# Performance work log

Hardware: AMD Instinct MI355X
Metric: run time of the kernel (lower is better)

Reference implementation:

```python
import jax, jax.numpy as jnp
import numpy as np


def _resize_hw(x, h, w):
    # PyTorch F.interpolate(mode='bilinear', align_corners=False) == half-pixel
    # bilinear without antialiasing.
    return jax.image.resize(x, x.shape[:-2] + (h, w), method='bilinear', antialias=False)


def _make_char_mask(attn, fore_mask, alpha):
    # attn: [b,26,w_attn] float; fore_mask: [b,1,H,W] int32
    W = fore_mask.shape[-1]
    attn_i = _resize_hw(attn[:, None], 26, W)[:, 0]          # [b,26,W]
    attn_b = (attn_i > alpha).astype(jnp.int32)              # threshold
    single = attn_b[:, :, None, :] * fore_mask               # [b,26,H,W]
    return jnp.concatenate([1 - fore_mask, single], axis=1)  # [b,27,H,W]


def _loss(char_feature, mask, length):
    # char_feature: [b,27,H,W] logits; mask: [b,27,H,W] int; length: [b]
    c = char_feature.shape[1]
    target = jnp.argmax(mask, axis=1)                         # [b,H,W] (first-max, same as torch)
    logp = jax.nn.log_softmax(char_feature, axis=1)
    ce = -jnp.mean(jnp.take_along_axis(logp, target[:, None], axis=1))
    prob = jnp.exp(logp)
    m = mask.astype(prob.dtype)
    smooth = 1.0
    inter = jnp.sum(prob * m, axis=(2, 3))                    # [b,27]
    s1 = jnp.sum(prob, axis=(2, 3))
    s2 = jnp.sum(m, axis=(2, 3))
    score = (2.0 * inter + smooth) / (s1 + s2 + smooth)       # [b,27]
    lens = length - 1                                          # chars per sample
    ch = jnp.arange(c)
    valid = (ch[None, :] >= 1) & (ch[None, :] <= lens[:, None])  # channels 1..len
    per_sample = jnp.sum((1.0 - score) * valid, axis=1) / lens.astype(prob.dtype)
    dice = jnp.mean(per_sample)
    return ce + dice


def setup_inputs() -> dict:
    key = jax.random.key(0)
    k1, k2, k3, k4, k5 = jax.random.split(key, 5)
    b = 512
    return {
        'char_feature_mid': jax.random.normal(k1, (b, 27, 32, 128), dtype=jnp.float32),
        'char_feature_low': jax.random.normal(k2, (b, 27, 16, 64), dtype=jnp.float32),
        'seq1_attention_map': jax.random.uniform(k3, (b, 26, 32), dtype=jnp.float32),
        'fore_mask': jax.random.uniform(k4, (b, 1, 32, 128), dtype=jnp.float32),
        'length': jax.random.randint(k5, (b,), 2, 27),
        'alpha': jnp.float32(0.3),
    }


def reference(char_feature_mid, char_feature_low, seq1_attention_map, fore_mask, length, alpha):
    h_mid, w_mid = char_feature_mid.shape[-2:]
    h_low, w_low = char_feature_low.shape[-2:]
    # clear_noise: zero attention rows at index >= length-1
    keep = jnp.arange(seq1_attention_map.shape[1])[None, :] < (length - 1)[:, None]
    attn = seq1_attention_map * keep[..., None].astype(seq1_attention_map.dtype)
    # low-resolution branch
    fm_low = (_resize_hw(fore_mask, h_low, w_low) >= 0.4).astype(jnp.int32)
    mask_low = _make_char_mask(attn, fm_low, alpha)
    loss_low = _loss(char_feature_low, mask_low, length)
    # middle-resolution branch
    fm_mid = (_resize_hw(fore_mask, h_mid, w_mid) >= 0.4).astype(jnp.int32)
    mask_mid = _make_char_mask(attn, fm_mid, alpha)
    loss_middle = _loss(char_feature_mid, mask_mid, length)
    return ((loss_low, loss_middle), mask_low)
```

## Files before the change

kernel.cpp:

```cpp
#include <hip/hip_runtime.h>
#include <stdint.h>


static __device__ __forceinline__ float wave_reduce_add(float v) {
  v += __shfl_xor(v, 1, 64);
  v += __shfl_xor(v, 2, 64);
  v += __shfl_xor(v, 4, 64);
  v += __shfl_xor(v, 8, 64);
  v += __shfl_xor(v, 16, 64);
  v += __shfl_xor(v, 32, 64);
  return v;
}

static __device__ __forceinline__ uint32_t attn_bits(const float* sattn, float src,
                                                     int lens, float alpha) {
  const int k0 = (int)floorf(src);
  uint32_t bits = 0u;
  if (k0 < 0 || k0 >= 31) {
    const int kk = (k0 < 0) ? 0 : 31;
    for (int c = 0; c < 26; ++c) {
      float v = (c < lens) ? sattn[c * 32 + kk] : 0.0f;
      if (v > alpha) bits |= (1u << c);
    }
  } else {
    const float frac = src - (float)k0;
    const float w1 = frac, w0 = 1.0f - frac;
    for (int c = 0; c < 26; ++c) {
      float v = __fadd_rn(__fmul_rn(w0, sattn[c * 32 + k0]),
                          __fmul_rn(w1, sattn[c * 32 + k0 + 1]));
      v = (c < lens) ? v : 0.0f;
      if (v > alpha) bits |= (1u << c);
    }
  }
  return bits;
}

__global__ __launch_bounds__(192) void prep_kernel(
    const float* __restrict__ attn,
    const int* __restrict__ length,
    const float* __restrict__ alpha_p,
    uint32_t* __restrict__ bits_mid,
    uint32_t* __restrict__ bits_low,
    float* __restrict__ acc_mid,
    float* __restrict__ acc_low,
    float* __restrict__ ce) {
  __shared__ float sattn[26 * 32];
  const int b = blockIdx.x;
  const int t = threadIdx.x;
  for (int i = t; i < 832; i += 192) sattn[i] = attn[b * 832 + i];
  if (t < 81) { acc_mid[b * 81 + t] = 0.0f; acc_low[b * 81 + t] = 0.0f; }
  if (b == 0 && t >= 96 && t < 98) ce[t - 96] = 0.0f;
  __syncthreads();
  const float alpha = alpha_p[0];
  const int lens = length[b] - 1;
  if (t < 128) {
    const float src = 0.25f * (float)t - 0.375f;
    bits_mid[b * 128 + t] = attn_bits(sattn, src, lens, alpha);
  } else {
    const int x = t - 128;
    const float src = 0.5f * (float)x - 0.25f;
    bits_low[b * 64 + x] = attn_bits(sattn, src, lens, alpha);
  }
}

__global__ __launch_bounds__(256) void main_kernel(
    const float* __restrict__ cf_mid,
    const float* __restrict__ cf_low,
    const float* __restrict__ fore,
    float* __restrict__ out,
    const uint32_t* __restrict__ bits_mid,
    const uint32_t* __restrict__ bits_low,
    float* __restrict__ acc_mid,
    float* __restrict__ acc_low,
    float* __restrict__ ce) {
  const int t = threadIdx.x;
  const int bid = blockIdx.x;
  const bool low = (bid >= 4096);
  int b, p0, W, HW;
  const float* cf;
  const uint32_t* bitsp;
  float* acc;
  if (low) {
    const int idx = bid - 4096;
    b = idx >> 1; p0 = (idx & 1) << 9; W = 64; HW = 1024;
    cf = cf_low; bitsp = bits_low + (size_t)b * 64; acc = acc_low;
  } else {
    b = bid >> 3; p0 = (bid & 7) << 9; W = 128; HW = 4096;
    cf = cf_mid; bitsp = bits_mid + (size_t)b * 128; acc = acc_mid;
  }
  const float* cfb = cf + (size_t)b * 27 * HW;
  const float* fb = fore + (size_t)b * 4096;
  float* mout = out + 2 + (size_t)b * 27 * 1024;

  float inter[27], s1[27], s2[27];
#pragma unroll
  for (int c = 0; c < 27; ++c) { inter[c] = 0.0f; s1[c] = 0.0f; s2[c] = 0.0f; }
  float cesum = 0.0f;

  for (int k = 0; k < 2; ++k) {
    const int p = p0 + t + (k << 8);
    const int x = p & (W - 1);

    int fmw;
    if (low) {
      const int y = p >> 6;
      const float2* fr = (const float2*)(fb + (size_t)(2 * y) * 128 + 2 * x);
      const float2 f0 = fr[0];
      const float2 f1 = fr[64];
      const float t0 = __fadd_rn(0.5f * f0.x, 0.5f * f1.x);
      const float t1 = __fadd_rn(0.5f * f0.y, 0.5f * f1.y);
      const float fmv = __fadd_rn(0.5f * t0, 0.5f * t1);
      fmw = (fmv >= 0.4f) ? 1 : 0;
    } else {
      fmw = (fb[p] >= 0.4f) ? 1 : 0;
    }

    const uint32_t bits = bitsp[x];
    const int target = fmw ? (int)__ffs(bits) : 0;

    float l[27];
    float m = -1e30f, lt = 0.0f;
#pragma unroll
    for (int c = 0; c < 27; ++c) {
      const float v = cfb[(size_t)c * HW + p];
      l[c] = v;
      m = fmaxf(m, v);
      lt = (c == target) ? v : lt;
    }
    float s = 0.0f;
#pragma unroll
    for (int c = 0; c < 27; ++c) {
      const float e = __expf(l[c] - m);
      l[c] = e;
      s += e;
    }
    const float inv = 1.0f / s;
    cesum += (m + __logf(s) - lt);

#pragma unroll
    for (int c = 0; c < 27; ++c) {
      const float prob = l[c] * inv;
      s1[c] += prob;
      float mf;
      if (c == 0) mf = (float)(1 - fmw);
      else mf = (float)(((bits >> (c - 1)) & 1u) & (uint32_t)fmw);
      inter[c] += prob * mf;
      s2[c] += mf;
      if (low) mout[(size_t)c * 1024 + p] = mf;
    }
  }

  __shared__ float red[4][82];
  const int wave = t >> 6, lane = t & 63;
#pragma unroll
  for (int c = 0; c < 27; ++c) {
    inter[c] = wave_reduce_add(inter[c]);
    s1[c] = wave_reduce_add(s1[c]);
    s2[c] = wave_reduce_add(s2[c]);
  }
  cesum = wave_reduce_add(cesum);
  if (lane == 0) {
#pragma unroll
    for (int c = 0; c < 27; ++c) {
      red[wave][c] = inter[c];
      red[wave][27 + c] = s1[c];
      red[wave][54 + c] = s2[c];
    }
    red[wave][81] = cesum;
  }
  __syncthreads();
  if (t < 82) {
    const float v = red[0][t] + red[1][t] + red[2][t] + red[3][t];
    if (t == 81) atomicAdd(&ce[low ? 0 : 1], v);
    else atomicAdd(&acc[(size_t)b * 81 + t], v);
  }
}

__global__ __launch_bounds__(256) void final_kernel(
    const float* __restrict__ acc_mid,
    const float* __restrict__ acc_low,
    const float* __restrict__ ce,
    const int* __restrict__ length,
    float* __restrict__ out) {
  const int B = blockIdx.x;
  const float* acc = (B == 0) ? acc_low : acc_mid;
  const float hw = (B == 0) ? 1024.0f : 4096.0f;
  const int t = threadIdx.x;
  float dsum = 0.0f;
  for (int b = t; b < 512; b += 256) {
    const int lens = length[b] - 1;
    const float* a = acc + (size_t)b * 81;
    float d = 0.0f;
    for (int c = 1; c < 27; ++c) {
      const float I = a[c], S1 = a[27 + c], S2 = a[54 + c];
      const float score = (2.0f * I + 1.0f) / (S1 + S2 + 1.0f);
      if (c <= lens) d += (1.0f - score);
    }
    dsum += d / (float)lens;
  }
  __shared__ float red[4];
  const int wave = t >> 6, lane = t & 63;
  dsum = wave_reduce_add(dsum);
  if (lane == 0) red[wave] = dsum;
  __syncthreads();
  if (t == 0) {
    const float dice = red[0] + red[1] + red[2] + red[3];
    out[B] = dice * (1.0f / 512.0f) + ce[B] * (1.0f / (512.0f * hw));
  }
}

extern "C" void kernel_launch(void* const* d_in, const int* in_sizes, int n_in,
                              void* d_out, int out_size, void* d_ws, size_t ws_size,
                              hipStream_t stream) {
  const float* cf_mid = (const float*)d_in[0];
  const float* cf_low = (const float*)d_in[1];
  const float* attn   = (const float*)d_in[2];
  const float* fore   = (const float*)d_in[3];
  const int*   length = (const int*)d_in[4];
  const float* alpha  = (const float*)d_in[5];
  float* out = (float*)d_out;

  uint32_t* bits_mid = (uint32_t*)d_ws;
  uint32_t* bits_low = bits_mid + 512 * 128;
  float* acc_mid = (float*)(bits_low + 512 * 64);
  float* acc_low = acc_mid + 512 * 81;
  float* ce = acc_low + 512 * 81;

  hipLaunchKernelGGL(prep_kernel, dim3(512), dim3(192), 0, stream,
                     attn, length, alpha, bits_mid, bits_low, acc_mid, acc_low, ce);
  hipLaunchKernelGGL(main_kernel, dim3(5120), dim3(256), 0, stream,
                     cf_mid, cf_low, fore, out, bits_mid, bits_low,
                     acc_mid, acc_low, ce);
  hipLaunchKernelGGL(final_kernel, dim3(2), dim3(256), 0, stream,
                     acc_mid, acc_low, ce, length, out);
}
```

Measured before the change: 411.0 us.

## Compute mask sums analytically in prep kernel and drop per-pixel s2 reduction

Since the attention mask is column-separable, the per-channel mask sums are computed in the prep kernel from per-column foreground counts and attention bits, and written directly into the accumulator. The main kernel no longer accumulates, wave-reduces or atomically adds 27 s2 values per block, which cuts register pressure and shuffle and atomic traffic. Launch bounds now request 4 blocks per CU. In exchange the prep kernel reads the full fore mask once more and does serial 128-element loops per channel.

```diff
diff --git a/kernel.cpp b/kernel.cpp
--- a/kernel.cpp
+++ b/kernel.cpp
@@ -37,6 +37,7 @@
 
 __global__ __launch_bounds__(192) void prep_kernel(
     const float* __restrict__ attn,
+    const float* __restrict__ fore,
     const int* __restrict__ length,
     const float* __restrict__ alpha_p,
     uint32_t* __restrict__ bits_mid,
@@ -45,25 +46,83 @@
     float* __restrict__ acc_low,
     float* __restrict__ ce) {
   __shared__ float sattn[26 * 32];
+  __shared__ int scnt_mid[128];
+  __shared__ int scnt_low[64];
+  __shared__ uint32_t sbits_mid[128];
+  __shared__ uint32_t sbits_low[64];
   const int b = blockIdx.x;
   const int t = threadIdx.x;
   for (int i = t; i < 832; i += 192) sattn[i] = attn[b * 832 + i];
-  if (t < 81) { acc_mid[b * 81 + t] = 0.0f; acc_low[b * 81 + t] = 0.0f; }
+  if (t < 54) { acc_mid[b * 81 + t] = 0.0f; acc_low[b * 81 + t] = 0.0f; }
   if (b == 0 && t >= 96 && t < 98) ce[t - 96] = 0.0f;
-  __syncthreads();
+
+  const float* fb = fore + (size_t)b * 4096;
+  if (t < 128) {
+    int cnt = 0;
+    for (int y = 0; y < 32; ++y) cnt += (fb[y * 128 + t] >= 0.4f) ? 1 : 0;
+    scnt_mid[t] = cnt;
+  } else {
+    const int x = t - 128;
+    int cnt = 0;
+    for (int y = 0; y < 16; ++y) {
+      const float2* fr = (const float2*)(fb + (size_t)(2 * y) * 128 + 2 * x);
+      const float2 f0 = fr[0];
+      const float2 f1 = fr[64];
+      const float t0 = __fadd_rn(0.5f * f0.x, 0.5f * f1.x);
+      const float t1 = __fadd_rn(0.5f * f0.y, 0.5f * f1.y);
+      const float fmv = __fadd_rn(0.5f * t0, 0.5f * t1);
+      cnt += (fmv >= 0.4f) ? 1 : 0;
+    }
+    scnt_low[x] = cnt;
+  }
+  __syncthreads();
+
   const float alpha = alpha_p[0];
   const int lens = length[b] - 1;
   if (t < 128) {
     const float src = 0.25f * (float)t - 0.375f;
-    bits_mid[b * 128 + t] = attn_bits(sattn, src, lens, alpha);
+    const uint32_t bits = attn_bits(sattn, src, lens, alpha);
+    bits_mid[b * 128 + t] = bits;
+    sbits_mid[t] = bits;
   } else {
     const int x = t - 128;
     const float src = 0.5f * (float)x - 0.25f;
-    bits_low[b * 64 + x] = attn_bits(sattn, src, lens, alpha);
-  }
-}
-
-__global__ __launch_bounds__(256) void main_kernel(
+    const uint32_t bits = attn_bits(sattn, src, lens, alpha);
+    bits_low[b * 64 + x] = bits;
+    sbits_low[x] = bits;
+  }
+  __syncthreads();
+
+  if (t < 27) {
+    const int c = t;
+    int s2;
+    if (c == 0) {
+      int tot = 0;
+      for (int x = 0; x < 128; ++x) tot += scnt_mid[x];
+      s2 = 4096 - tot;
+    } else {
+      s2 = 0;
+      for (int x = 0; x < 128; ++x)
+        s2 += (int)((sbits_mid[x] >> (c - 1)) & 1u) * scnt_mid[x];
+    }
+    acc_mid[b * 81 + 54 + c] = (float)s2;
+  } else if (t >= 64 && t < 91) {
+    const int c = t - 64;
+    int s2;
+    if (c == 0) {
+      int tot = 0;
+      for (int x = 0; x < 64; ++x) tot += scnt_low[x];
+      s2 = 1024 - tot;
+    } else {
+      s2 = 0;
+      for (int x = 0; x < 64; ++x)
+        s2 += (int)((sbits_low[x] >> (c - 1)) & 1u) * scnt_low[x];
+    }
+    acc_low[b * 81 + 54 + c] = (float)s2;
+  }
+}
+
+__global__ __launch_bounds__(256, 4) void main_kernel(
     const float* __restrict__ cf_mid,
     const float* __restrict__ cf_low,
     const float* __restrict__ fore,
@@ -92,9 +151,9 @@
   const float* fb = fore + (size_t)b * 4096;
   float* mout = out + 2 + (size_t)b * 27 * 1024;
 
-  float inter[27], s1[27], s2[27];
-#pragma unroll
-  for (int c = 0; c < 27; ++c) { inter[c] = 0.0f; s1[c] = 0.0f; s2[c] = 0.0f; }
+  float inter[27], s1[27];
+#pragma unroll
+  for (int c = 0; c < 27; ++c) { inter[c] = 0.0f; s1[c] = 0.0f; }
   float cesum = 0.0f;
 
   for (int k = 0; k < 2; ++k) {
@@ -145,18 +204,16 @@
       if (c == 0) mf = (float)(1 - fmw);
       else mf = (float)(((bits >> (c - 1)) & 1u) & (uint32_t)fmw);
       inter[c] += prob * mf;
-      s2[c] += mf;
       if (low) mout[(size_t)c * 1024 + p] = mf;
     }
   }
 
-  __shared__ float red[4][82];
+  __shared__ float red[4][55];
   const int wave = t >> 6, lane = t & 63;
 #pragma unroll
   for (int c = 0; c < 27; ++c) {
     inter[c] = wave_reduce_add(inter[c]);
     s1[c] = wave_reduce_add(s1[c]);
-    s2[c] = wave_reduce_add(s2[c]);
   }
   cesum = wave_reduce_add(cesum);
   if (lane == 0) {
@@ -164,14 +221,13 @@
     for (int c = 0; c < 27; ++c) {
       red[wave][c] = inter[c];
       red[wave][27 + c] = s1[c];
-      red[wave][54 + c] = s2[c];
-    }
-    red[wave][81] = cesum;
-  }
-  __syncthreads();
-  if (t < 82) {
+    }
+    red[wave][54] = cesum;
+  }
+  __syncthreads();
+  if (t < 55) {
     const float v = red[0][t] + red[1][t] + red[2][t] + red[3][t];
-    if (t == 81) atomicAdd(&ce[low ? 0 : 1], v);
+    if (t == 54) atomicAdd(&ce[low ? 0 : 1], v);
     else atomicAdd(&acc[(size_t)b * 81 + t], v);
   }
 }
@@ -227,7 +283,8 @@
   float* ce = acc_low + 512 * 81;
 
   hipLaunchKernelGGL(prep_kernel, dim3(512), dim3(192), 0, stream,
-                     attn, length, alpha, bits_mid, bits_low, acc_mid, acc_low, ce);
+                     attn, fore, length, alpha, bits_mid, bits_low,
+                     acc_mid, acc_low, ce);
   hipLaunchKernelGGL(main_kernel, dim3(5120), dim3(256), 0, stream,
                      cf_mid, cf_low, fore, out, bits_mid, bits_low,
                      acc_mid, acc_low, ce);
```

Result: slower. 539.0 us (+31.2%).
